# Kernel tuning notes

Measured on AMD Instinct MI355X. Metric: run time of the kernel, lower is better.

## Reference

```python
import jax, jax.numpy as jnp
import numpy as np

N, E, M = 100000, 3200000, 1000000  # nodes, message edges, scored move edges
DIN, H = 128, 64


def setup_inputs() -> dict:
    key = jax.random.key(0)
    ks = jax.random.split(key, 20)
    rn = lambda k, shape, s=0.05: (jax.random.normal(k, shape, jnp.float32) * s)
    return {
        "x": jax.random.normal(ks[0], (N, DIN), jnp.float32),
        "edge_index": jax.random.randint(ks[1], (2, E), 0, N, jnp.int64),
        "move_edge_index": jax.random.randint(ks[2], (2, M), 0, N, jnp.int64),
        "lin1_w": rn(ks[3], (DIN, H)), "lin1_b": jnp.zeros((H,), jnp.float32),
        "lin2_w": rn(ks[4], (H, H)), "lin2_b": jnp.zeros((H,), jnp.float32),
        "conv1_wl": rn(ks[5], (H, H)), "conv1_bl": jnp.zeros((H,), jnp.float32),
        "conv1_wr": rn(ks[6], (H, H)),
        "conv2_wl": rn(ks[7], (H, H)), "conv2_bl": jnp.zeros((H,), jnp.float32),
        "conv2_wr": rn(ks[8], (H, H)),
        "mlp_w1": rn(ks[9], (2 * H, H)), "mlp_b1": jnp.zeros((H,), jnp.float32),
        "mlp_w2": rn(ks[10], (H, 1)), "mlp_b2": jnp.zeros((1,), jnp.float32),
    }


def reference(x, edge_index, move_edge_index,
              lin1_w, lin1_b, lin2_w, lin2_b,
              conv1_wl, conv1_bl, conv1_wr,
              conv2_wl, conv2_bl, conv2_wr,
              mlp_w1, mlp_b1, mlp_w2, mlp_b2):
    n = x.shape[0]
    src, dst = edge_index[0], edge_index[1]
    # mean-aggregation degrees (PyG SAGEConv default aggr='mean'; isolated nodes -> 0)
    deg = jax.ops.segment_sum(jnp.ones(src.shape, x.dtype), dst, num_segments=n)
    inv_deg = (jnp.where(deg > 0, 1.0 / jnp.maximum(deg, 1.0), 0.0))[:, None]

    def sage(h, wl, bl, wr):
        # out = W_l @ mean_j h_j + b_l + W_r @ h_i
        agg = jax.ops.segment_sum(h[src], dst, num_segments=n) * inv_deg
        return agg @ wl + bl + h @ wr

    h = jax.nn.relu(x @ lin1_w + lin1_b)
    h = jax.nn.relu(sage(h, conv1_wl, conv1_bl, conv1_wr))
    h = jax.nn.relu(h @ lin2_w + lin2_b)
    h = jax.nn.relu(sage(h, conv2_wl, conv2_bl, conv2_wr))

    # edge scoring: gather src/dst embeddings, concat, 2-layer MLP, tanh
    cat = jnp.concatenate([h[move_edge_index[0]], h[move_edge_index[1]]], axis=1)  # [M, 2H]
    logits = (jax.nn.relu(cat @ mlp_w1 + mlp_b1) @ mlp_w2 + mlp_b2).reshape(-1)
    return jnp.tanh(logits)
```

## Files before the change

kernel.cpp:

```cpp
#include <hip/hip_runtime.h>
#include <math.h>

#define MAXB 512
#define PART_BS 1024
#define CAPB 256

typedef _Float16 f16;
typedef __attribute__((ext_vector_type(2))) _Float16 f16x2;
typedef __attribute__((ext_vector_type(4))) _Float16 f16x4;
typedef __attribute__((ext_vector_type(8))) _Float16 f16x8;
typedef __attribute__((ext_vector_type(4))) float f32x4;

static __device__ __forceinline__ unsigned short f2h(float f) {
    f16 h = (f16)f; return *(unsigned short*)&h;
}

__global__ __launch_bounds__(PART_BS) void k_part(const int* __restrict__ src,
                                                  const int* __restrict__ dst,
                                                  unsigned* __restrict__ bb,
                                                  int* __restrict__ cnt,
                                                  int E, int shift, int pcap,
                                                  int nblk, int nb) {
    __shared__ int h[MAXB];
    const int blk = blockIdx.x;
    const int b0 = blk * pcap;
    const int e1 = min(b0 + pcap, E);
    for (int i = threadIdx.x; i < MAXB; i += PART_BS) h[i] = 0;
    __syncthreads();
    const unsigned mask = (1u << shift) - 1u;
    for (int pos = b0 + (int)threadIdx.x * 8; pos < e1; pos += PART_BS * 8) {
        if (pos + 8 <= e1) {
            int4 d0 = *(const int4*)(dst + pos), d1 = *(const int4*)(dst + pos + 4);
            int4 s0 = *(const int4*)(src + pos), s1 = *(const int4*)(src + pos + 4);
            int dd[8] = {d0.x, d0.y, d0.z, d0.w, d1.x, d1.y, d1.z, d1.w};
            int ss[8] = {s0.x, s0.y, s0.z, s0.w, s1.x, s1.y, s1.z, s1.w};
#pragma unroll
            for (int k = 0; k < 8; ++k) {
                int b = dd[k] >> shift;
                int r = atomicAdd(&h[b], 1);
                if (r < CAPB)
                    bb[((size_t)b * nblk + blk) * CAPB + r] =
                        ((unsigned)ss[k] << shift) | ((unsigned)dd[k] & mask);
            }
        } else {
            for (int k = 0; pos + k < e1; ++k) {
                int d = dst[pos + k];
                int b = d >> shift;
                int r = atomicAdd(&h[b], 1);
                if (r < CAPB)
                    bb[((size_t)b * nblk + blk) * CAPB + r] =
                        ((unsigned)src[pos + k] << shift) | ((unsigned)d & mask);
            }
        }
    }
    __syncthreads();
    for (int i = threadIdx.x; i < nb; i += PART_BS)
        cnt[(size_t)i * nblk + blk] = min(h[i], CAPB);
}

__global__ __launch_bounds__(512) void k_bfill(const unsigned* __restrict__ bb,
                                               const int* __restrict__ cnt,
                                               int* __restrict__ row_st,
                                               int* __restrict__ row_en,
                                               float* __restrict__ inv_deg,
                                               int* __restrict__ csr,
                                               int N, int shift, int CAP, int nblk) {
    __shared__ int deg[512], cur[512], s[512];
    __shared__ int scnt[1024];
    int b = blockIdx.x;
    int t = threadIdx.x;
    int lo = b << shift;
    int hi = min(N, (b + 1) << shift);
    int nn = hi - lo;
    unsigned off = (unsigned)b * CAP;
    unsigned mask = (1u << shift) - 1u;
    const unsigned* seg = bb + (size_t)b * nblk * CAPB;

    for (int i = t; i < nblk; i += 512) scnt[i] = cnt[(size_t)b * nblk + i];
    deg[t] = 0;
    __syncthreads();
    const int tot = nblk * CAPB;
    for (int i = t; i < tot; i += 512)
        if ((i & (CAPB - 1)) < scnt[i >> 8])
            atomicAdd(&deg[seg[i] & mask], 1);
    __syncthreads();
    int d = deg[t];
    int pd = (d + 31) & ~31;
    s[t] = pd;
    __syncthreads();
    for (int o = 1; o < 512; o <<= 1) {
        int u = (t >= o) ? s[t - o] : 0;
        __syncthreads();
        s[t] += u;
        __syncthreads();
    }
    int excl = min(s[t] - pd, CAP);
    int pe = min(excl + pd, CAP);
    cur[t] = excl;
    if (t < nn) {
        row_st[lo + t] = (int)off + excl;
        row_en[lo + t] = (int)off + pe;
        inv_deg[lo + t] = d > 0 ? 1.0f / (float)d : 0.0f;
        for (int j = excl + d; j < pe; ++j) csr[off + j] = N;
    }
    __syncthreads();
    for (int i = t; i < tot; i += 512)
        if ((i & (CAPB - 1)) < scnt[i >> 8]) {
            unsigned w = seg[i];
            int dl = (int)(w & mask);
            int pos = atomicAdd(&cur[dl], 1);
            if (pos < CAP) csr[off + pos] = (int)(w >> shift);
        }
}

__global__ __launch_bounds__(256) void k_prep(
    const float* __restrict__ lin1_w, const float* __restrict__ c1_wl,
    const float* __restrict__ c1_wr, const float* __restrict__ lin2_w,
    const float* __restrict__ c2_wl, const float* __restrict__ c2_wr,
    const float* __restrict__ mlp_w1, const float* __restrict__ mlp_w2,
    unsigned short* __restrict__ Wt) {
    int i = blockIdx.x * 256 + threadIdx.x;
    for (; i < 36928; i += gridDim.x * 256) {
        float v;
        if (i < 8192)       { int j = i;         int n = j >> 7, k = j & 127; v = lin1_w[k * 64 + n]; }
        else if (i < 16384) { int j = i - 8192;  int n = j >> 7, k = j & 127;
                              v = (k < 64) ? c1_wl[k * 64 + n] : c1_wr[(k - 64) * 64 + n]; }
        else if (i < 20480) { int j = i - 16384; int n = j >> 6, k = j & 63;  v = lin2_w[k * 64 + n]; }
        else if (i < 28672) { int j = i - 20480; int n = j >> 7, k = j & 127;
                              v = (k < 64) ? c2_wl[k * 64 + n] : c2_wr[(k - 64) * 64 + n]; }
        else if (i < 32768) { int j = i - 28672; int n = j >> 6, k = j & 63;  v = mlp_w1[k * 64 + n]; }
        else if (i < 36864) { int j = i - 32768; int n = j >> 6, k = j & 63;  v = mlp_w1[(k + 64) * 64 + n]; }
        else                { v = mlp_w2[i - 36864]; }
        Wt[i] = f2h(v);
    }
}

__global__ __launch_bounds__(256) void k_gather_h(
    const _Float16* __restrict__ hh, const int* __restrict__ csr,
    const int* __restrict__ row_st, const int* __restrict__ row_en,
    const float* __restrict__ inv_deg, _Float16* __restrict__ out, int n) {
    int node = (blockIdx.x * 256 + (int)threadIdx.x) >> 6;
    if (node >= n) return;
    int lane = threadIdx.x & 63;
    int g = lane >> 3, sub = lane & 7;
    int base = row_st[node], end = row_en[node];
    float a[8] = {0.f, 0.f, 0.f, 0.f, 0.f, 0.f, 0.f, 0.f};
#if __has_builtin(__builtin_amdgcn_fdot2)
    const f16x2 one2 = {(f16)1.f, (f16)1.f};
#endif
    for (; base + 64 <= end; base += 64) {
        int4 sA = *(const int4*)&csr[base + 4 * g];
        int4 sB = *(const int4*)&csr[base + 32 + 4 * g];
        int sidx[8] = {sA.x, sA.y, sA.z, sA.w, sB.x, sB.y, sB.z, sB.w};
        f16x8 u[8];
#pragma unroll
        for (int t = 0; t < 8; ++t)
            u[t] = *(const f16x8*)(hh + (((unsigned)sidx[t] << 6) + ((unsigned)sub << 3)));
#if __has_builtin(__builtin_amdgcn_fdot2)
#pragma unroll
        for (int t = 0; t < 8; t += 2)
#pragma unroll
            for (int j = 0; j < 8; ++j) {
                f16x2 v = {u[t][j], u[t + 1][j]};
                a[j] = __builtin_amdgcn_fdot2(v, one2, a[j], false);
            }
#else
#pragma unroll
        for (int t = 0; t < 8; ++t)
#pragma unroll
            for (int j = 0; j < 8; ++j) a[j] += (float)u[t][j];
#endif
    }
    if (base < end) {
        int4 sA = *(const int4*)&csr[base + 4 * g];
        int sidx[4] = {sA.x, sA.y, sA.z, sA.w};
        f16x8 u[4];
#pragma unroll
        for (int t = 0; t < 4; ++t)
            u[t] = *(const f16x8*)(hh + (((unsigned)sidx[t] << 6) + ((unsigned)sub << 3)));
#if __has_builtin(__builtin_amdgcn_fdot2)
#pragma unroll
        for (int t = 0; t < 4; t += 2)
#pragma unroll
            for (int j = 0; j < 8; ++j) {
                f16x2 v = {u[t][j], u[t + 1][j]};
                a[j] = __builtin_amdgcn_fdot2(v, one2, a[j], false);
            }
#else
#pragma unroll
        for (int t = 0; t < 4; ++t)
#pragma unroll
            for (int j = 0; j < 8; ++j) a[j] += (float)u[t][j];
#endif
    }
#pragma unroll
    for (int j = 0; j < 8; ++j) {
        a[j] += __shfl_xor(a[j], 8, 64);
        a[j] += __shfl_xor(a[j], 16, 64);
        a[j] += __shfl_xor(a[j], 32, 64);
    }
    if (g == 0) {
        float idv = inv_deg[node];
        f16x8 o;
#pragma unroll
        for (int j = 0; j < 8; ++j) o[j] = (f16)(a[j] * idv);
        *(f16x8*)(out + (((unsigned)node << 6) + ((unsigned)sub << 3))) = o;
    }
}

__global__ __launch_bounds__(256) void k_mm1(
    const float* __restrict__ x, const unsigned short* __restrict__ Wtg,
    const float* __restrict__ bias, unsigned short* __restrict__ outh, int n) {
    __shared__ alignas(16) unsigned short sW[64 * 136];
    const int tid = threadIdx.x;
    const int row0 = blockIdx.x * 64;
    if (blockIdx.x == 0 && tid < 8)
        ((uint4*)(outh + (size_t)n * 64))[tid] = (uint4){0, 0, 0, 0};
    for (int i = tid; i < 64 * 16; i += 256) {
        int nn = i >> 4, c = i & 15;
        *(uint4*)&sW[(nn * 17 + c) * 8] = *(const uint4*)&Wtg[i * 8];
    }
    __syncthreads();
    const int lane = tid & 63, w = tid >> 6;
    const int m = lane & 15, q = lane >> 4;
    const int gr = min(row0 + 16 * w + m, n - 1);
    const float* ar = x + (size_t)gr * 128;
    f32x4 acc[4];
#pragma unroll
    for (int c = 0; c < 4; ++c) acc[c] = (f32x4){0.f, 0.f, 0.f, 0.f};
#pragma unroll
    for (int kk = 0; kk < 4; ++kk) {
        float4 a0 = *(const float4*)(ar + kk * 32 + q * 8);
        float4 a1 = *(const float4*)(ar + kk * 32 + q * 8 + 4);
        f16x8 af;
        af[0] = (f16)a0.x; af[1] = (f16)a0.y; af[2] = (f16)a0.z; af[3] = (f16)a0.w;
        af[4] = (f16)a1.x; af[5] = (f16)a1.y; af[6] = (f16)a1.z; af[7] = (f16)a1.w;
#pragma unroll
        for (int c = 0; c < 4; ++c) {
            f16x8 bf = *(const f16x8*)&sW[((16 * c + m) * 17 + (kk * 4 + q)) * 8];
            acc[c] = __builtin_amdgcn_mfma_f32_16x16x32_f16(af, bf, acc[c], 0, 0, 0);
        }
    }
#pragma unroll
    for (int c = 0; c < 4; ++c) {
        int col = 16 * c + m;
        float bv = bias[col];
#pragma unroll
        for (int i = 0; i < 4; ++i) {
            int r = row0 + 16 * w + q * 4 + i;
            if (r < n) outh[(size_t)r * 64 + col] = f2h(fmaxf(acc[c][i] + bv, 0.f));
        }
    }
}

__global__ __launch_bounds__(256) void k_mm23(
    const unsigned short* __restrict__ aggH, const unsigned short* __restrict__ h1,
    const unsigned short* __restrict__ Wcg, const float* __restrict__ bl,
    const unsigned short* __restrict__ Wl2g, const float* __restrict__ b2,
    unsigned short* __restrict__ outh, int n) {
    __shared__ alignas(16) unsigned short sm[64 * 72 + 64 * 136];
    unsigned short* hA = sm;
    unsigned short* sW = sm + 64 * 72;
    const int tid = threadIdx.x;
    const int row0 = blockIdx.x * 64;
    for (int i = tid; i < 64 * 16; i += 256) {
        int nn = i >> 4, c = i & 15;
        *(uint4*)&sW[(nn * 17 + c) * 8] = *(const uint4*)&Wcg[i * 8];
    }
    __syncthreads();
    const int lane = tid & 63, w = tid >> 6;
    const int m = lane & 15, q = lane >> 4;
    const int gr = min(row0 + 16 * w + m, n - 1);
    f32x4 acc[4];
#pragma unroll
    for (int c = 0; c < 4; ++c) acc[c] = (f32x4){0.f, 0.f, 0.f, 0.f};
#pragma unroll
    for (int kk = 0; kk < 4; ++kk) {
        const unsigned short* ap = (kk < 2)
            ? (aggH + (size_t)gr * 64 + kk * 32 + q * 8)
            : (h1 + (size_t)gr * 64 + (kk - 2) * 32 + q * 8);
        f16x8 af = *(const f16x8*)ap;
#pragma unroll
        for (int c = 0; c < 4; ++c) {
            f16x8 bf = *(const f16x8*)&sW[((16 * c + m) * 17 + (kk * 4 + q)) * 8];
            acc[c] = __builtin_amdgcn_mfma_f32_16x16x32_f16(af, bf, acc[c], 0, 0, 0);
        }
    }
#pragma unroll
    for (int c = 0; c < 4; ++c) {
        int col = 16 * c + m;
        float bv = bl[col];
#pragma unroll
        for (int i = 0; i < 4; ++i)
            hA[(16 * w + q * 4 + i) * 72 + col] = f2h(fmaxf(acc[c][i] + bv, 0.f));
    }
    __syncthreads();
    for (int i = tid; i < 64 * 8; i += 256) {
        int nn = i >> 3, c = i & 7;
        *(uint4*)&sW[(nn * 9 + c) * 8] = *(const uint4*)&Wl2g[i * 8];
    }
    __syncthreads();
    f32x4 acc2[4];
#pragma unroll
    for (int c = 0; c < 4; ++c) acc2[c] = (f32x4){0.f, 0.f, 0.f, 0.f};
#pragma unroll
    for (int kk = 0; kk < 2; ++kk) {
        f16x8 af = *(const f16x8*)&hA[(16 * w + m) * 72 + kk * 32 + q * 8];
#pragma unroll
        for (int c = 0; c < 4; ++c) {
            f16x8 bf = *(const f16x8*)&sW[((16 * c + m) * 9 + (kk * 4 + q)) * 8];
            acc2[c] = __builtin_amdgcn_mfma_f32_16x16x32_f16(af, bf, acc2[c], 0, 0, 0);
        }
    }
#pragma unroll
    for (int c = 0; c < 4; ++c) {
        int col = 16 * c + m;
        float bv = b2[col];
#pragma unroll
        for (int i = 0; i < 4; ++i) {
            int r = row0 + 16 * w + q * 4 + i;
            if (r < n) outh[(size_t)r * 64 + col] = f2h(fmaxf(acc2[c][i] + bv, 0.f));
        }
    }
}

__global__ __launch_bounds__(256) void k_mm456(
    const unsigned short* __restrict__ aggH, const unsigned short* __restrict__ h3,
    const unsigned short* __restrict__ Wcg, const float* __restrict__ bl,
    const unsigned short* __restrict__ Wpg, const unsigned short* __restrict__ Wqg,
    const float* __restrict__ b1, unsigned short* __restrict__ Ph,
    unsigned short* __restrict__ Qh, int n) {
    __shared__ alignas(16) unsigned short sm[64 * 72 + 2 * 64 * 72];
    unsigned short* hA = sm;
    unsigned short* sW = sm + 64 * 72;
    const int tid = threadIdx.x;
    const int row0 = blockIdx.x * 64;
    for (int i = tid; i < 64 * 16; i += 256) {
        int nn = i >> 4, c = i & 15;
        *(uint4*)&sW[(nn * 17 + c) * 8] = *(const uint4*)&Wcg[i * 8];
    }
    __syncthreads();
    const int lane = tid & 63, w = tid >> 6;
    const int m = lane & 15, q = lane >> 4;
    const int gr = min(row0 + 16 * w + m, n - 1);
    f32x4 acc[4];
#pragma unroll
    for (int c = 0; c < 4; ++c) acc[c] = (f32x4){0.f, 0.f, 0.f, 0.f};
#pragma unroll
    for (int kk = 0; kk < 4; ++kk) {
        const unsigned short* ap = (kk < 2)
            ? (aggH + (size_t)gr * 64 + kk * 32 + q * 8)
            : (h3 + (size_t)gr * 64 + (kk - 2) * 32 + q * 8);
        f16x8 af = *(const f16x8*)ap;
#pragma unroll
        for (int c = 0; c < 4; ++c) {
            f16x8 bf = *(const f16x8*)&sW[((16 * c + m) * 17 + (kk * 4 + q)) * 8];
            acc[c] = __builtin_amdgcn_mfma_f32_16x16x32_f16(af, bf, acc[c], 0, 0, 0);
        }
    }
#pragma unroll
    for (int c = 0; c < 4; ++c) {
        int col = 16 * c + m;
        float bv = bl[col];
#pragma unroll
        for (int i = 0; i < 4; ++i)
            hA[(16 * w + q * 4 + i) * 72 + col] = f2h(fmaxf(acc[c][i] + bv, 0.f));
    }
    __syncthreads();
    for (int i = tid; i < 64 * 8; i += 256) {
        int nn = i >> 3, c = i & 7;
        *(uint4*)&sW[(nn * 9 + c) * 8] = *(const uint4*)&Wpg[i * 8];
        *(uint4*)&sW[4608 + (nn * 9 + c) * 8] = *(const uint4*)&Wqg[i * 8];
    }
    __syncthreads();
    f32x4 accP[4], accQ[4];
#pragma unroll
    for (int c = 0; c < 4; ++c) {
        accP[c] = (f32x4){0.f, 0.f, 0.f, 0.f};
        accQ[c] = (f32x4){0.f, 0.f, 0.f, 0.f};
    }
#pragma unroll
    for (int kk = 0; kk < 2; ++kk) {
        f16x8 af = *(const f16x8*)&hA[(16 * w + m) * 72 + kk * 32 + q * 8];
#pragma unroll
        for (int c = 0; c < 4; ++c) {
            f16x8 bp = *(const f16x8*)&sW[((16 * c + m) * 9 + (kk * 4 + q)) * 8];
            f16x8 bq = *(const f16x8*)&sW[4608 + ((16 * c + m) * 9 + (kk * 4 + q)) * 8];
            accP[c] = __builtin_amdgcn_mfma_f32_16x16x32_f16(af, bp, accP[c], 0, 0, 0);
            accQ[c] = __builtin_amdgcn_mfma_f32_16x16x32_f16(af, bq, accQ[c], 0, 0, 0);
        }
    }
#pragma unroll
    for (int c = 0; c < 4; ++c) {
        int col = 16 * c + m;
        float bv = b1[col];
#pragma unroll
        for (int i = 0; i < 4; ++i) {
            int r = row0 + 16 * w + q * 4 + i;
            if (r < n) {
                Ph[(size_t)r * 64 + col] = f2h(accP[c][i] + bv);
                Qh[(size_t)r * 64 + col] = f2h(accQ[c][i]);
            }
        }
    }
}

__global__ __launch_bounds__(256) void k_score_h(
    const _Float16* __restrict__ P, const _Float16* __restrict__ Q,
    const int* __restrict__ msrc, const int* __restrict__ mdst,
    const _Float16* __restrict__ w2h, const float* __restrict__ b2,
    float* __restrict__ out, int M) {
    int gid = blockIdx.x * 256 + threadIdx.x;
    int e = gid >> 3;
    if (e >= M) return;
    int l = gid & 7;
    int s = msrc[e], d = mdst[e];
    f16x8 p = *(const f16x8*)(P + (((unsigned)s << 6) + ((unsigned)l << 3)));
    f16x8 q = *(const f16x8*)(Q + (((unsigned)d << 6) + ((unsigned)l << 3)));
    f16x8 w = *(const f16x8*)(w2h + ((unsigned)l << 3));
    f16x8 u = p + q;
    f16x8 z = {(f16)0, (f16)0, (f16)0, (f16)0, (f16)0, (f16)0, (f16)0, (f16)0};
    u = __builtin_elementwise_max(u, z);
    float partial;
#if __has_builtin(__builtin_amdgcn_fdot2)
    f16x2 u01 = {u[0], u[1]}, u23 = {u[2], u[3]}, u45 = {u[4], u[5]}, u67 = {u[6], u[7]};
    f16x2 w01 = {w[0], w[1]}, w23 = {w[2], w[3]}, w45 = {w[4], w[5]}, w67 = {w[6], w[7]};
    partial = __builtin_amdgcn_fdot2(u01, w01,
              __builtin_amdgcn_fdot2(u23, w23,
              __builtin_amdgcn_fdot2(u45, w45,
              __builtin_amdgcn_fdot2(u67, w67, 0.f, false), false), false), false);
#else
    partial = 0.f;
#pragma unroll
    for (int i = 0; i < 8; ++i) partial += (float)u[i] * (float)w[i];
#endif
    partial += __shfl_xor(partial, 1, 8);
    partial += __shfl_xor(partial, 2, 8);
    partial += __shfl_xor(partial, 4, 8);
    if (l == 0) {
        float xx = partial + b2[0];
        float t = __expf(2.f * xx);
        out[e] = (t - 1.f) / (t + 1.f);
    }
}

extern "C" void kernel_launch(void* const* d_in, const int* in_sizes, int n_in,
                              void* d_out, int out_size, void* d_ws, size_t ws_size,
                              hipStream_t stream) {
    const float* x      = (const float*)d_in[0];
    const int*   ei     = (const int*)d_in[1];
    const int*   mei    = (const int*)d_in[2];
    const float* lin1_w = (const float*)d_in[3];
    const float* lin1_b = (const float*)d_in[4];
    const float* lin2_w = (const float*)d_in[5];
    const float* lin2_b = (const float*)d_in[6];
    const float* c1_wl  = (const float*)d_in[7];
    const float* c1_bl  = (const float*)d_in[8];
    const float* c1_wr  = (const float*)d_in[9];
    const float* c2_wl  = (const float*)d_in[10];
    const float* c2_bl  = (const float*)d_in[11];
    const float* c2_wr  = (const float*)d_in[12];
    const float* mlp_w1 = (const float*)d_in[13];
    const float* mlp_b1 = (const float*)d_in[14];
    const float* mlp_w2 = (const float*)d_in[15];
    const float* mlp_b2 = (const float*)d_in[16];

    const int N = in_sizes[0] / 128;
    const int E = in_sizes[1] / 2;
    const int M = in_sizes[2] / 2;
    const int* src  = ei;
    const int* dstE = ei + E;
    const int* msrc = mei;
    const int* mdst = mei + M;

    int shift = 8;
    while ((((N - 1) >> shift) + 1) > MAXB) ++shift;
    const int nbuckets = ((N - 1) >> shift) + 1;
    long long avg = (((long long)E << shift) / N) + 1;
    int CAP = (int)((2 * avg + 2047) & ~1023LL);

    const size_t N64 = (size_t)N * 64;
    const size_t aliasBytes = (3 * N64 + 64) * 2;
    int pcap = 32768;
    int nblk = (E + pcap - 1) / pcap;
    while ((size_t)nblk * nbuckets * CAPB * 4 > aliasBytes || nblk > 1024) {
        pcap <<= 1;
        nblk = (E + pcap - 1) / pcap;
    }

    unsigned short* Hh   = (unsigned short*)d_ws;
    unsigned short* aggH = Hh + N64 + 64;
    unsigned short* Qh   = aggH + N64;
    float* inv_deg = (float*)(Qh + N64);
    int*   row_st  = (int*)(inv_deg + N);
    int*   row_en  = row_st + N;
    int*   cnt     = row_en + N;
    unsigned short* Wt = (unsigned short*)(cnt + (size_t)nbuckets * nblk);
    int*   csr     = (int*)(Wt + 36928 + 32);
    unsigned* bb   = (unsigned*)Hh;
    float* outf = (float*)d_out;

    const int nbN = (N + 63) / 64;
    const int nbM = (int)(((long long)M * 8 + 255) / 256);
    const int nbG = (int)(((long long)N * 64 + 255) / 256);

    k_prep<<<64, 256, 0, stream>>>(lin1_w, c1_wl, c1_wr, lin2_w, c2_wl, c2_wr,
                                   mlp_w1, mlp_w2, Wt);
    k_part<<<nblk, PART_BS, 0, stream>>>(src, dstE, bb, cnt, E, shift, pcap,
                                         nblk, nbuckets);
    k_bfill<<<nbuckets, 512, 0, stream>>>(bb, cnt, row_st, row_en,
                                          inv_deg, csr, N, shift, CAP, nblk);

    k_mm1<<<nbN, 256, 0, stream>>>(x, Wt + 0, lin1_b, Hh, N);

    k_gather_h<<<nbG, 256, 0, stream>>>((const _Float16*)Hh, csr, row_st, row_en,
                                        inv_deg, (_Float16*)aggH, N);
    k_mm23<<<nbN, 256, 0, stream>>>(aggH, Hh, Wt + 8192, c1_bl,
                                    Wt + 16384, lin2_b, Hh, N);

    k_gather_h<<<nbG, 256, 0, stream>>>((const _Float16*)Hh, csr, row_st, row_en,
                                        inv_deg, (_Float16*)aggH, N);
    k_mm456<<<nbN, 256, 0, stream>>>(aggH, Hh, Wt + 20480, c2_bl,
                                     Wt + 28672, Wt + 32768, mlp_b1,
                                     Hh, Qh, N);

    k_score_h<<<nbM, 256, 0, stream>>>((const _Float16*)Hh, (const _Float16*)Qh,
                                       msrc, mdst, (const _Float16*)(Wt + 36864),
                                       mlp_b2, outf, M);
}
```

Measured before the change: 412.3 us.

## Replace bucketed two-pass CSR build with global-atomic degree, scan, scatter

Drops the shared-memory bucket partition and per-bucket fill kernels. Degrees are now counted with global atomics, per-node row offsets are assigned through a block scan plus one global atomic base, and edges are scattered into the CSR with global atomics on per-node cursors. This removes the intermediate bucket buffer, the capacity limits and the fixed per-bucket CSR regions. In exchange it adds many contended global atomics and random scattered writes over 3.2M edges. Row order across blocks becomes nondeterministic, which only affects summation order.

```diff
diff --git a/kernel.cpp b/kernel.cpp
--- a/kernel.cpp
+++ b/kernel.cpp
@@ -1,9 +1,5 @@
 #include <hip/hip_runtime.h>
 #include <math.h>
-
-#define MAXB 512
-#define PART_BS 1024
-#define CAPB 256
 
 typedef _Float16 f16;
 typedef __attribute__((ext_vector_type(2))) _Float16 f16x2;
@@ -15,102 +11,58 @@
     f16 h = (f16)f; return *(unsigned short*)&h;
 }
 
-__global__ __launch_bounds__(PART_BS) void k_part(const int* __restrict__ src,
-                                                  const int* __restrict__ dst,
-                                                  unsigned* __restrict__ bb,
-                                                  int* __restrict__ cnt,
-                                                  int E, int shift, int pcap,
-                                                  int nblk, int nb) {
-    __shared__ int h[MAXB];
-    const int blk = blockIdx.x;
-    const int b0 = blk * pcap;
-    const int e1 = min(b0 + pcap, E);
-    for (int i = threadIdx.x; i < MAXB; i += PART_BS) h[i] = 0;
-    __syncthreads();
-    const unsigned mask = (1u << shift) - 1u;
-    for (int pos = b0 + (int)threadIdx.x * 8; pos < e1; pos += PART_BS * 8) {
-        if (pos + 8 <= e1) {
-            int4 d0 = *(const int4*)(dst + pos), d1 = *(const int4*)(dst + pos + 4);
-            int4 s0 = *(const int4*)(src + pos), s1 = *(const int4*)(src + pos + 4);
-            int dd[8] = {d0.x, d0.y, d0.z, d0.w, d1.x, d1.y, d1.z, d1.w};
-            int ss[8] = {s0.x, s0.y, s0.z, s0.w, s1.x, s1.y, s1.z, s1.w};
-#pragma unroll
-            for (int k = 0; k < 8; ++k) {
-                int b = dd[k] >> shift;
-                int r = atomicAdd(&h[b], 1);
-                if (r < CAPB)
-                    bb[((size_t)b * nblk + blk) * CAPB + r] =
-                        ((unsigned)ss[k] << shift) | ((unsigned)dd[k] & mask);
-            }
-        } else {
-            for (int k = 0; pos + k < e1; ++k) {
-                int d = dst[pos + k];
-                int b = d >> shift;
-                int r = atomicAdd(&h[b], 1);
-                if (r < CAPB)
-                    bb[((size_t)b * nblk + blk) * CAPB + r] =
-                        ((unsigned)src[pos + k] << shift) | ((unsigned)d & mask);
-            }
-        }
-    }
-    __syncthreads();
-    for (int i = threadIdx.x; i < nb; i += PART_BS)
-        cnt[(size_t)i * nblk + blk] = min(h[i], CAPB);
-}
-
-__global__ __launch_bounds__(512) void k_bfill(const unsigned* __restrict__ bb,
-                                               const int* __restrict__ cnt,
-                                               int* __restrict__ row_st,
-                                               int* __restrict__ row_en,
-                                               float* __restrict__ inv_deg,
-                                               int* __restrict__ csr,
-                                               int N, int shift, int CAP, int nblk) {
-    __shared__ int deg[512], cur[512], s[512];
-    __shared__ int scnt[1024];
-    int b = blockIdx.x;
+__global__ __launch_bounds__(256) void k_deg(const int* __restrict__ dst,
+                                             int* __restrict__ deg, int E) {
+    int i = blockIdx.x * 256 + threadIdx.x;
+    int stride = gridDim.x * 256;
+    for (int p = i; p < E; p += stride)
+        atomicAdd(&deg[dst[p]], 1);
+}
+
+__global__ __launch_bounds__(256) void k_rows(const int* __restrict__ deg,
+                                              int* __restrict__ gtot,
+                                              int* __restrict__ row_st,
+                                              int* __restrict__ row_en,
+                                              int* __restrict__ cur,
+                                              float* __restrict__ inv_deg,
+                                              int* __restrict__ csr, int N) {
+    __shared__ int s[256];
+    __shared__ int basesh;
     int t = threadIdx.x;
-    int lo = b << shift;
-    int hi = min(N, (b + 1) << shift);
-    int nn = hi - lo;
-    unsigned off = (unsigned)b * CAP;
-    unsigned mask = (1u << shift) - 1u;
-    const unsigned* seg = bb + (size_t)b * nblk * CAPB;
-
-    for (int i = t; i < nblk; i += 512) scnt[i] = cnt[(size_t)b * nblk + i];
-    deg[t] = 0;
-    __syncthreads();
-    const int tot = nblk * CAPB;
-    for (int i = t; i < tot; i += 512)
-        if ((i & (CAPB - 1)) < scnt[i >> 8])
-            atomicAdd(&deg[seg[i] & mask], 1);
-    __syncthreads();
-    int d = deg[t];
+    int node = blockIdx.x * 256 + t;
+    int d = (node < N) ? deg[node] : 0;
     int pd = (d + 31) & ~31;
     s[t] = pd;
     __syncthreads();
-    for (int o = 1; o < 512; o <<= 1) {
+    for (int o = 1; o < 256; o <<= 1) {
         int u = (t >= o) ? s[t - o] : 0;
         __syncthreads();
         s[t] += u;
         __syncthreads();
     }
-    int excl = min(s[t] - pd, CAP);
-    int pe = min(excl + pd, CAP);
-    cur[t] = excl;
-    if (t < nn) {
-        row_st[lo + t] = (int)off + excl;
-        row_en[lo + t] = (int)off + pe;
-        inv_deg[lo + t] = d > 0 ? 1.0f / (float)d : 0.0f;
-        for (int j = excl + d; j < pe; ++j) csr[off + j] = N;
-    }
-    __syncthreads();
-    for (int i = t; i < tot; i += 512)
-        if ((i & (CAPB - 1)) < scnt[i >> 8]) {
-            unsigned w = seg[i];
-            int dl = (int)(w & mask);
-            int pos = atomicAdd(&cur[dl], 1);
-            if (pos < CAP) csr[off + pos] = (int)(w >> shift);
-        }
+    if (t == 255) basesh = atomicAdd(gtot, s[255]);
+    __syncthreads();
+    int excl = basesh + s[t] - pd;
+    if (node < N) {
+        row_st[node] = excl;
+        row_en[node] = excl + pd;
+        cur[node] = excl;
+        inv_deg[node] = d > 0 ? 1.0f / (float)d : 0.0f;
+        for (int j = d; j < pd; ++j) csr[excl + j] = N;
+    }
+}
+
+__global__ __launch_bounds__(256) void k_scatter(const int* __restrict__ src,
+                                                 const int* __restrict__ dst,
+                                                 int* __restrict__ cur,
+                                                 int* __restrict__ csr, int E) {
+    int i = blockIdx.x * 256 + threadIdx.x;
+    int stride = gridDim.x * 256;
+    for (int p = i; p < E; p += stride) {
+        int d = dst[p];
+        int pos = atomicAdd(&cur[d], 1);
+        csr[pos] = src[p];
+    }
 }
 
 __global__ __launch_bounds__(256) void k_prep(
@@ -473,43 +425,32 @@
     const int* msrc = mei;
     const int* mdst = mei + M;
 
-    int shift = 8;
-    while ((((N - 1) >> shift) + 1) > MAXB) ++shift;
-    const int nbuckets = ((N - 1) >> shift) + 1;
-    long long avg = (((long long)E << shift) / N) + 1;
-    int CAP = (int)((2 * avg + 2047) & ~1023LL);
-
     const size_t N64 = (size_t)N * 64;
-    const size_t aliasBytes = (3 * N64 + 64) * 2;
-    int pcap = 32768;
-    int nblk = (E + pcap - 1) / pcap;
-    while ((size_t)nblk * nbuckets * CAPB * 4 > aliasBytes || nblk > 1024) {
-        pcap <<= 1;
-        nblk = (E + pcap - 1) / pcap;
-    }
-
     unsigned short* Hh   = (unsigned short*)d_ws;
     unsigned short* aggH = Hh + N64 + 64;
     unsigned short* Qh   = aggH + N64;
     float* inv_deg = (float*)(Qh + N64);
     int*   row_st  = (int*)(inv_deg + N);
     int*   row_en  = row_st + N;
-    int*   cnt     = row_en + N;
-    unsigned short* Wt = (unsigned short*)(cnt + (size_t)nbuckets * nblk);
+    int*   cur     = row_en + N;
+    int*   deg     = cur + N;
+    unsigned short* Wt = (unsigned short*)(deg + N + 8);
     int*   csr     = (int*)(Wt + 36928 + 32);
-    unsigned* bb   = (unsigned*)Hh;
     float* outf = (float*)d_out;
 
     const int nbN = (N + 63) / 64;
     const int nbM = (int)(((long long)M * 8 + 255) / 256);
     const int nbG = (int)(((long long)N * 64 + 255) / 256);
-
+    const int nbE = min(2048, (E + 255) / 256);
+    const int nbR = (N + 255) / 256;
+
+    hipMemsetAsync(deg, 0, (size_t)(N + 1) * sizeof(int), stream);
     k_prep<<<64, 256, 0, stream>>>(lin1_w, c1_wl, c1_wr, lin2_w, c2_wl, c2_wr,
                                    mlp_w1, mlp_w2, Wt);
-    k_part<<<nblk, PART_BS, 0, stream>>>(src, dstE, bb, cnt, E, shift, pcap,
-                                         nblk, nbuckets);
-    k_bfill<<<nbuckets, 512, 0, stream>>>(bb, cnt, row_st, row_en,
-                                          inv_deg, csr, N, shift, CAP, nblk);
+    k_deg<<<nbE, 256, 0, stream>>>(dstE, deg, E);
+    k_rows<<<nbR, 256, 0, stream>>>(deg, deg + N, row_st, row_en, cur,
+                                    inv_deg, csr, N);
+    k_scatter<<<nbE, 256, 0, stream>>>(src, dstE, cur, csr, E);
 
     k_mm1<<<nbN, 256, 0, stream>>>(x, Wt + 0, lin1_b, Hh, N);
 
```

New measurement: 730.9 us. 1.77x slower.
